# Kernel tuning notes

Measured on AMD Instinct MI355X. Metric: run time of the kernel, lower is better.

## Reference

```python
import jax, jax.numpy as jnp
import numpy as np

NUM_LAYERS = 2


def _relabel(sig, order_pos, M):
    """Assign consecutive int ids to unique rows of sig [M, K], numbered by
    first occurrence according to order_pos (mimics torch dict-insertion order)."""
    # lexsort: primary key must be last -> reverse columns
    perm = jnp.lexsort(tuple(sig[:, ::-1].T))
    s = sig[perm]
    neq = jnp.any(s[1:] != s[:-1], axis=1)
    gid_sorted = jnp.concatenate(
        [jnp.zeros(1, jnp.int32), jnp.cumsum(neq).astype(jnp.int32)])
    gid = jnp.zeros(M, jnp.int32).at[perm].set(gid_sorted)
    # first occurrence position of each group (empty segments -> int32 max)
    first = jax.ops.segment_min(order_pos, gid, num_segments=M)
    order = jnp.argsort(first)  # groups ranked by first occurrence
    ranks = jnp.zeros(M, jnp.int32).at[order].set(jnp.arange(M, dtype=jnp.int32))
    return ranks[gid]


def _histogram(labels, M):
    # torch returns length == num_colors; we pad with zeros to the static max M
    return jnp.zeros(M, jnp.int32).at[labels.reshape(-1)].add(1)


def setup_inputs() -> dict:
    key = jax.random.key(0)
    k1, k2 = jax.random.split(key)
    N, E, C = 256, 8192, 16
    x = jax.random.randint(k1, (N,), 0, C, dtype=jnp.int32)
    edge_index = jax.random.randint(k2, (2, E), 0, N, dtype=jnp.int32)
    return {"x": x, "edge_index": edge_index}


def reference(x, edge_index):
    x = x.astype(jnp.int32)
    N = x.shape[0]
    M = N * N
    # adjacency indicator (duplicate edges collapse, matching the any() check)
    A = jnp.zeros((N, N), jnp.int32).at[edge_index[0], edge_index[1]].set(1)

    # atomic coloring: signature = (x[v1], x[v2], connected)
    sig0 = jnp.stack([
        jnp.broadcast_to(x[:, None], (N, N)).reshape(M),
        jnp.broadcast_to(x[None, :], (N, N)).reshape(M),
        A.reshape(M),
    ], axis=1)
    # torch iterates permutations (i!=j, lexicographic) first, then the diagonal
    i = jnp.arange(N, dtype=jnp.int32)[:, None]
    j = jnp.arange(N, dtype=jnp.int32)[None, :]
    off = i * (N - 1) + jnp.where(j < i, j, j - 1)
    pos = jnp.where(i == j, N * (N - 1) + i, off).reshape(M)
    labels = _relabel(sig0, pos, M).reshape(N, N)

    hists = [_histogram(labels, M)]
    rowmajor = jnp.arange(M, dtype=jnp.int32)
    for _ in range(NUM_LAYERS):
        row_s = jnp.sort(labels, axis=1)        # sorted row multiset per v1
        col_s = jnp.sort(labels, axis=0).T      # sorted col multiset per v2
        sig = jnp.concatenate([
            labels.reshape(M, 1),
            jnp.broadcast_to(row_s[:, None, :], (N, N, N)).reshape(M, N),
            jnp.broadcast_to(col_s[None, :, :], (N, N, N)).reshape(M, N),
        ], axis=1)  # [M, 2N+1]
        labels = _relabel(sig, rowmajor, M).reshape(N, N)
        hists.append(_histogram(labels, M))
    return tuple(hists)
```

## Files before the change

kernel.cpp:

```cpp
#include <hip/hip_runtime.h>

#define NN 256
#define MM 65536
#define TBL 131072
#define TBL_MASK (TBL - 1)

__device__ __forceinline__ unsigned key0m(const int* x, const int* A, int i, int j, int m) {
    return ((unsigned)x[i] << 5) | ((unsigned)x[j] << 1) | (unsigned)A[m];
}

__device__ __forceinline__ unsigned long long mix64(unsigned v) {
    unsigned long long z = (unsigned long long)v + 0x9E3779B97F4A7C15ull;
    z = (z ^ (z >> 30)) * 0xBF58476D1CE4E5B9ull;
    z = (z ^ (z >> 27)) * 0x94D049BB133111EBull;
    return z ^ (z >> 31);
}


__global__ void build_adj(const int* __restrict__ ei, int* __restrict__ A, int E) {
    int e = blockIdx.x * blockDim.x + threadIdx.x;
    if (e < E) {
        int s = ei[e];
        int d = ei[E + e];
        A[s * NN + d] = 1;
    }
}

__global__ void init_key_pass(const int* __restrict__ x, const int* __restrict__ A,
                              unsigned* __restrict__ mp0, unsigned* __restrict__ c0,
                              int* __restrict__ hist0) {
    int m = blockIdx.x * blockDim.x + threadIdx.x;
    hist0[m] = 0;
    int i = m >> 8, j = m & 255;
    unsigned key = key0m(x, A, i, j, m);
    unsigned pos = (i == j) ? (unsigned)(NN * (NN - 1) + i)
                            : (unsigned)(i * (NN - 1) + (j < i ? j : j - 1));
    atomicMax(&mp0[key], ~pos);
    atomicAdd(&c0[key], 1u);
}

__global__ void rank0_fused(const unsigned* __restrict__ mp0, const unsigned* __restrict__ c0,
                            unsigned* __restrict__ rank0, int* __restrict__ hist) {
    __shared__ unsigned pos_s[512];
    int k = threadIdx.x;
    unsigned c = c0[k];
    pos_s[k] = c ? ~mp0[k] : 0xFFFFFFFFu;
    __syncthreads();
    if (c) {
        unsigned my = pos_s[k];
        int rk = 0;
        for (int kk = 0; kk < 512; ++kk) rk += (pos_s[kk] < my);
        rank0[k] = (unsigned)rk;
        hist[rk] = (int)c;
    }
}

__global__ void hash_both(const int* __restrict__ x, const int* __restrict__ A,
                          const unsigned* __restrict__ rank0, const int* __restrict__ lab,
                          int layer, unsigned long long* __restrict__ rowhash,
                          unsigned long long* __restrict__ colhash) {
    __shared__ unsigned long long hs[256];
    int b = blockIdx.x, t = threadIdx.x;
    int i = b & 255, mode = b >> 8;
    int m = mode ? t * NN + i : i * NN + t;
    unsigned lv = (layer == 0)
                      ? rank0[key0m(x, A, mode ? t : i, mode ? i : t, m)]
                      : (unsigned)lab[m];
    hs[t] = mix64(lv);
    __syncthreads();
    for (int off = 128; off > 0; off >>= 1) {
        if (t < off) hs[t] += hs[t + off];
        __syncthreads();
    }
    if (t == 0) (mode ? colhash : rowhash)[i] = hs[0];
}

__global__ void rep_hash(const unsigned long long* __restrict__ rowhash,
                         const unsigned long long* __restrict__ colhash,
                         int* __restrict__ rvec, int* __restrict__ cvec) {
    __shared__ unsigned long long hh[512];
    int t = threadIdx.x;
    hh[t] = (t < 256) ? rowhash[t] : colhash[t - 256];
    __syncthreads();
    int mode = t >> 8, i = t & 255, base = mode << 8;
    unsigned long long my = hh[base + i];
    int r = i;
    for (int j = 0; j < i; ++j) {
        if (hh[base + j] == my) {
            r = j;
            break;
        }
    }
    (mode ? cvec : rvec)[i] = r;
}

__global__ void relabel_insert(const int* __restrict__ x, const int* __restrict__ A,
                               const unsigned* __restrict__ rank0, const int* __restrict__ lab,
                               int layer, const int* __restrict__ r, const int* __restrict__ c,
                               unsigned long long* __restrict__ tk, unsigned* __restrict__ mp,
                               unsigned* __restrict__ cnt, unsigned* __restrict__ slotidx) {
    int m = blockIdx.x * blockDim.x + threadIdx.x;
    int i = m >> 8, j = m & 255;
    unsigned l = (layer == 0) ? rank0[key0m(x, A, i, j, m)] : (unsigned)lab[m];
    unsigned key = l | ((unsigned)r[i] << 16) | ((unsigned)c[j] << 24);
    unsigned long long kk = (unsigned long long)key + 1ull;
    unsigned h = ((key * 2654435761u) >> 15) & TBL_MASK;
    for (;;) {
        unsigned long long prev = atomicCAS(&tk[h], 0ull, kk);
        if (prev == 0ull || prev == kk) break;
        h = (h + 1) & TBL_MASK;
    }
    slotidx[m] = h;
    atomicMax(&mp[h], ~(unsigned)m);
    atomicAdd(&cnt[h], 1u);
}

__global__ void mark_bm(const unsigned long long* __restrict__ tk,
                        const unsigned* __restrict__ mp, unsigned* __restrict__ bm,
                        int* __restrict__ hist) {
    int s = blockIdx.x * blockDim.x + threadIdx.x;
    if (s < MM) hist[s] = 0;
    if (tk[s]) {
        unsigned q = ~mp[s];
        atomicOr(&bm[q >> 5], 1u << (q & 31));
    }
}

__global__ void finish_bm(const unsigned long long* __restrict__ tk,
                          const unsigned* __restrict__ mp, const unsigned* __restrict__ cnt,
                          const unsigned* __restrict__ bm, const unsigned* __restrict__ slotidx,
                          int* __restrict__ hist, int* __restrict__ lab) {
    __shared__ unsigned bw[2048];
    __shared__ unsigned wb[2048];
    __shared__ unsigned ts[256];
    int t = threadIdx.x;
    for (int k = t; k < 2048; k += 256) bw[k] = bm[k];
    __syncthreads();
    unsigned pc[8], s = 0;
#pragma unroll
    for (int k = 0; k < 8; ++k) {
        pc[k] = (unsigned)__popc(bw[t * 8 + k]);
        s += pc[k];
    }
    ts[t] = s;
    __syncthreads();
    for (int off = 1; off < 256; off <<= 1) {
        unsigned v = (t >= off) ? ts[t - off] : 0u;
        __syncthreads();
        ts[t] += v;
        __syncthreads();
    }
    unsigned run = ts[t] - s;
#pragma unroll
    for (int k = 0; k < 8; ++k) {
        wb[t * 8 + k] = run;
        run += pc[k];
    }
    __syncthreads();

    int sdx = blockIdx.x * 256 + t;
    if (sdx < MM) {
        unsigned q = ~mp[slotidx[sdx]];
        lab[sdx] = (int)(wb[q >> 5] + (unsigned)__popc(bw[q >> 5] & ((1u << (q & 31)) - 1u)));
    }
    if (tk[sdx]) {
        unsigned q = ~mp[sdx];
        unsigned rk = wb[q >> 5] + (unsigned)__popc(bw[q >> 5] & ((1u << (q & 31)) - 1u));
        hist[rk] = (int)cnt[sdx];
    }
}

extern "C" void kernel_launch(void* const* d_in, const int* in_sizes, int n_in,
                              void* d_out, int out_size, void* d_ws, size_t ws_size,
                              hipStream_t stream) {
    const int* x = (const int*)d_in[0];
    const int* ei = (const int*)d_in[1];
    const int E = in_sizes[1] / 2;
    int* out = (int*)d_out;

    char* w = (char*)d_ws;
    size_t off = 0;
    auto alloc = [&](size_t bytes) -> void* {
        void* p = w + off;
        off = (off + bytes + 511) & ~(size_t)511;
        return p;
    };
    unsigned long long* tkL[2] = {(unsigned long long*)alloc(TBL * 8),
                                  (unsigned long long*)alloc(TBL * 8)};
    unsigned* mpL[2] = {(unsigned*)alloc(TBL * 4), (unsigned*)alloc(TBL * 4)};
    unsigned* cntL[2] = {(unsigned*)alloc(TBL * 4), (unsigned*)alloc(TBL * 4)};
    unsigned* bmL[2] = {(unsigned*)alloc(2048 * 4), (unsigned*)alloc(2048 * 4)};
    int* A = (int*)alloc(MM * 4);
    unsigned* mp0 = (unsigned*)alloc(512 * 4);
    unsigned* c0 = (unsigned*)alloc(512 * 4);
    size_t zero_end = off;
    unsigned* slotidx = (unsigned*)alloc(MM * 4);
    int* lab = (int*)alloc(MM * 4);
    unsigned long long* rowhash = (unsigned long long*)alloc(NN * 8);
    unsigned long long* colhash = (unsigned long long*)alloc(NN * 8);
    int* rvec = (int*)alloc(NN * 4);
    int* cvec = (int*)alloc(NN * 4);
    unsigned* rank0 = (unsigned*)alloc(512 * 4);

    (void)hipMemsetAsync(d_ws, 0, zero_end, stream);

    build_adj<<<(E + 255) / 256, 256, 0, stream>>>(ei, A, E);
    init_key_pass<<<MM / 256, 256, 0, stream>>>(x, A, mp0, c0, out);
    rank0_fused<<<1, 512, 0, stream>>>(mp0, c0, rank0, out);

    for (int layer = 0; layer < 2; ++layer) {
        int* hist = out + (size_t)(layer + 1) * MM;
        hash_both<<<2 * NN, NN, 0, stream>>>(x, A, rank0, lab, layer, rowhash, colhash);
        rep_hash<<<1, 512, 0, stream>>>(rowhash, colhash, rvec, cvec);
        relabel_insert<<<MM / 256, 256, 0, stream>>>(x, A, rank0, lab, layer, rvec, cvec,
                                                     tkL[layer], mpL[layer], cntL[layer],
                                                     slotidx);
        mark_bm<<<TBL / 256, 256, 0, stream>>>(tkL[layer], mpL[layer], bmL[layer], hist);
        finish_bm<<<TBL / 256, 256, 0, stream>>>(tkL[layer], mpL[layer], cntL[layer], bmL[layer],
                                                 slotidx, hist, lab);
    }
}
```

Before: 200.5 us.

## Use bitmask adjacency, fuse memset with adjacency build, fold rep_hash into insert

```diff
diff --git a/kernel.cpp b/kernel.cpp
--- a/kernel.cpp
+++ b/kernel.cpp
@@ -5,8 +5,13 @@
 #define TBL 131072
 #define TBL_MASK (TBL - 1)
 
-__device__ __forceinline__ unsigned key0m(const int* x, const int* A, int i, int j, int m) {
-    return ((unsigned)x[i] << 5) | ((unsigned)x[j] << 1) | (unsigned)A[m];
+__device__ __forceinline__ unsigned abit(const unsigned* Abm, int m) {
+    return (Abm[m >> 5] >> (m & 31)) & 1u;
+}
+
+__device__ __forceinline__ unsigned key0b(const int* x, const unsigned* Abm, int i, int j,
+                                          int m) {
+    return ((unsigned)x[i] << 5) | ((unsigned)x[j] << 1) | abit(Abm, m);
 }
 
 __device__ __forceinline__ unsigned long long mix64(unsigned v) {
@@ -16,23 +21,35 @@
     return z ^ (z >> 31);
 }
 
-
-__global__ void build_adj(const int* __restrict__ ei, int* __restrict__ A, int E) {
-    int e = blockIdx.x * blockDim.x + threadIdx.x;
-    if (e < E) {
-        int s = ei[e];
-        int d = ei[E + e];
-        A[s * NN + d] = 1;
-    }
-}
-
-__global__ void init_key_pass(const int* __restrict__ x, const int* __restrict__ A,
-                              unsigned* __restrict__ mp0, unsigned* __restrict__ c0,
-                              int* __restrict__ hist0) {
-    int m = blockIdx.x * blockDim.x + threadIdx.x;
+__global__ void adj_zero(const int* __restrict__ ei, int E, unsigned* __restrict__ Abm,
+                         uint4* __restrict__ zdst, unsigned nzq4) {
+    int b = blockIdx.x, t = threadIdx.x;
+    if (b == 0) {
+        __shared__ unsigned abm_s[2048];
+        for (int k = t; k < 2048; k += 256) abm_s[k] = 0u;
+        __syncthreads();
+        for (int e = t; e < E; e += 256) {
+            int s = ei[e], d = ei[E + e];
+            int m = s * NN + d;
+            atomicOr(&abm_s[m >> 5], 1u << (m & 31));
+        }
+        __syncthreads();
+        for (int k = t; k < 2048; k += 256) Abm[k] = abm_s[k];
+    } else {
+        uint4 z;
+        z.x = z.y = z.z = z.w = 0u;
+        for (unsigned q = (unsigned)(b - 1) * 256u + (unsigned)t; q < nzq4; q += 511u * 256u)
+            zdst[q] = z;
+    }
+}
+
+__global__ void init_key(const int* __restrict__ x, const unsigned* __restrict__ Abm,
+                         unsigned* __restrict__ mp0, unsigned* __restrict__ c0,
+                         int* __restrict__ hist0) {
+    int m = blockIdx.x * 256 + threadIdx.x;
     hist0[m] = 0;
     int i = m >> 8, j = m & 255;
-    unsigned key = key0m(x, A, i, j, m);
+    unsigned key = key0b(x, Abm, i, j, m);
     unsigned pos = (i == j) ? (unsigned)(NN * (NN - 1) + i)
                             : (unsigned)(i * (NN - 1) + (j < i ? j : j - 1));
     atomicMax(&mp0[key], ~pos);
@@ -55,7 +72,7 @@
     }
 }
 
-__global__ void hash_both(const int* __restrict__ x, const int* __restrict__ A,
+__global__ void hash_both(const int* __restrict__ x, const unsigned* __restrict__ Abm,
                           const unsigned* __restrict__ rank0, const int* __restrict__ lab,
                           int layer, unsigned long long* __restrict__ rowhash,
                           unsigned long long* __restrict__ colhash) {
@@ -64,7 +81,7 @@
     int i = b & 255, mode = b >> 8;
     int m = mode ? t * NN + i : i * NN + t;
     unsigned lv = (layer == 0)
-                      ? rank0[key0m(x, A, mode ? t : i, mode ? i : t, m)]
+                      ? rank0[key0b(x, Abm, mode ? t : i, mode ? i : t, m)]
                       : (unsigned)lab[m];
     hs[t] = mix64(lv);
     __syncthreads();
@@ -75,34 +92,47 @@
     if (t == 0) (mode ? colhash : rowhash)[i] = hs[0];
 }
 
-__global__ void rep_hash(const unsigned long long* __restrict__ rowhash,
-                         const unsigned long long* __restrict__ colhash,
-                         int* __restrict__ rvec, int* __restrict__ cvec) {
-    __shared__ unsigned long long hh[512];
-    int t = threadIdx.x;
-    hh[t] = (t < 256) ? rowhash[t] : colhash[t - 256];
-    __syncthreads();
-    int mode = t >> 8, i = t & 255, base = mode << 8;
-    unsigned long long my = hh[base + i];
-    int r = i;
-    for (int j = 0; j < i; ++j) {
-        if (hh[base + j] == my) {
-            r = j;
-            break;
+__global__ void insert_rep(const int* __restrict__ x, const unsigned* __restrict__ Abm,
+                           const unsigned* __restrict__ rank0, const int* __restrict__ lab,
+                           int layer, const unsigned long long* __restrict__ rowhash,
+                           const unsigned long long* __restrict__ colhash,
+                           unsigned long long* __restrict__ tk, unsigned* __restrict__ mp,
+                           unsigned* __restrict__ cnt, unsigned* __restrict__ slotidx) {
+    __shared__ unsigned long long rh[256];
+    __shared__ unsigned long long ch[256];
+    __shared__ int cvec_s[256];
+    __shared__ int rvec_b;
+    int b = blockIdx.x, t = threadIdx.x;
+    rh[t] = rowhash[t];
+    ch[t] = colhash[t];
+    __syncthreads();
+    {
+        unsigned long long my = ch[t];
+        int r = t;
+        for (int j = 0; j < t; ++j) {
+            if (ch[j] == my) {
+                r = j;
+                break;
+            }
         }
-    }
-    (mode ? cvec : rvec)[i] = r;
-}
-
-__global__ void relabel_insert(const int* __restrict__ x, const int* __restrict__ A,
-                               const unsigned* __restrict__ rank0, const int* __restrict__ lab,
-                               int layer, const int* __restrict__ r, const int* __restrict__ c,
-                               unsigned long long* __restrict__ tk, unsigned* __restrict__ mp,
-                               unsigned* __restrict__ cnt, unsigned* __restrict__ slotidx) {
-    int m = blockIdx.x * blockDim.x + threadIdx.x;
-    int i = m >> 8, j = m & 255;
-    unsigned l = (layer == 0) ? rank0[key0m(x, A, i, j, m)] : (unsigned)lab[m];
-    unsigned key = l | ((unsigned)r[i] << 16) | ((unsigned)c[j] << 24);
+        cvec_s[t] = r;
+    }
+    if (t == 0) {
+        unsigned long long my = rh[b];
+        int r = b;
+        for (int j = 0; j < b; ++j) {
+            if (rh[j] == my) {
+                r = j;
+                break;
+            }
+        }
+        rvec_b = r;
+    }
+    __syncthreads();
+
+    int m = b * 256 + t;
+    unsigned l = (layer == 0) ? rank0[key0b(x, Abm, b, t, m)] : (unsigned)lab[m];
+    unsigned key = l | ((unsigned)rvec_b << 16) | ((unsigned)cvec_s[t] << 24);
     unsigned long long kk = (unsigned long long)key + 1ull;
     unsigned h = ((key * 2654435761u) >> 15) & TBL_MASK;
     for (;;) {
@@ -118,7 +148,7 @@
 __global__ void mark_bm(const unsigned long long* __restrict__ tk,
                         const unsigned* __restrict__ mp, unsigned* __restrict__ bm,
                         int* __restrict__ hist) {
-    int s = blockIdx.x * blockDim.x + threadIdx.x;
+    int s = blockIdx.x * 256 + threadIdx.x;
     if (s < MM) hist[s] = 0;
     if (tk[s]) {
         unsigned q = ~mp[s];
@@ -185,12 +215,13 @@
         off = (off + bytes + 511) & ~(size_t)511;
         return p;
     };
+    unsigned* Abm = (unsigned*)alloc(2048 * 4);
+    size_t zero_begin = off;
     unsigned long long* tkL[2] = {(unsigned long long*)alloc(TBL * 8),
                                   (unsigned long long*)alloc(TBL * 8)};
     unsigned* mpL[2] = {(unsigned*)alloc(TBL * 4), (unsigned*)alloc(TBL * 4)};
     unsigned* cntL[2] = {(unsigned*)alloc(TBL * 4), (unsigned*)alloc(TBL * 4)};
     unsigned* bmL[2] = {(unsigned*)alloc(2048 * 4), (unsigned*)alloc(2048 * 4)};
-    int* A = (int*)alloc(MM * 4);
     unsigned* mp0 = (unsigned*)alloc(512 * 4);
     unsigned* c0 = (unsigned*)alloc(512 * 4);
     size_t zero_end = off;
@@ -198,23 +229,19 @@
     int* lab = (int*)alloc(MM * 4);
     unsigned long long* rowhash = (unsigned long long*)alloc(NN * 8);
     unsigned long long* colhash = (unsigned long long*)alloc(NN * 8);
-    int* rvec = (int*)alloc(NN * 4);
-    int* cvec = (int*)alloc(NN * 4);
     unsigned* rank0 = (unsigned*)alloc(512 * 4);
 
-    (void)hipMemsetAsync(d_ws, 0, zero_end, stream);
-
-    build_adj<<<(E + 255) / 256, 256, 0, stream>>>(ei, A, E);
-    init_key_pass<<<MM / 256, 256, 0, stream>>>(x, A, mp0, c0, out);
+    unsigned nzq4 = (unsigned)((zero_end - zero_begin) / 16);
+
+    adj_zero<<<512, 256, 0, stream>>>(ei, E, Abm, (uint4*)(w + zero_begin), nzq4);
+    init_key<<<MM / 256, 256, 0, stream>>>(x, Abm, mp0, c0, out);
     rank0_fused<<<1, 512, 0, stream>>>(mp0, c0, rank0, out);
 
     for (int layer = 0; layer < 2; ++layer) {
         int* hist = out + (size_t)(layer + 1) * MM;
-        hash_both<<<2 * NN, NN, 0, stream>>>(x, A, rank0, lab, layer, rowhash, colhash);
-        rep_hash<<<1, 512, 0, stream>>>(rowhash, colhash, rvec, cvec);
-        relabel_insert<<<MM / 256, 256, 0, stream>>>(x, A, rank0, lab, layer, rvec, cvec,
-                                                     tkL[layer], mpL[layer], cntL[layer],
-                                                     slotidx);
+        hash_both<<<2 * NN, NN, 0, stream>>>(x, Abm, rank0, lab, layer, rowhash, colhash);
+        insert_rep<<<MM / 256, 256, 0, stream>>>(x, Abm, rank0, lab, layer, rowhash, colhash,
+                                                 tkL[layer], mpL[layer], cntL[layer], slotidx);
         mark_bm<<<TBL / 256, 256, 0, stream>>>(tkL[layer], mpL[layer], bmL[layer], hist);
         finish_bm<<<TBL / 256, 256, 0, stream>>>(tkL[layer], mpL[layer], cntL[layer], bmL[layer],
                                                  slotidx, hist, lab);
```

After: 208.4 us. +3.9%, slower.
